# Optimization experiments

Measured on AMD Instinct MI355X. Metric: run time of the kernel, lower is better.

Reference implementation:

```python
import jax, jax.numpy as jnp
import numpy as np

EMBED_DIM = 1024
NUM_HEADS = 16
HEAD_DIM = EMBED_DIM // NUM_HEADS


def setup_inputs() -> dict:
    key = jax.random.key(0)
    k_x, k_wqkv, k_bqkv, k_wo, k_bo = jax.random.split(key, 5)
    B, T, C = 8, 1024, EMBED_DIM
    s = 1.0 / np.sqrt(C)
    return {
        "x": jax.random.normal(k_x, (B, T, C), dtype=jnp.float32),
        "W_qkv": jax.random.uniform(k_wqkv, (C, 3 * C), minval=-s, maxval=s, dtype=jnp.float32),
        "b_qkv": jax.random.uniform(k_bqkv, (3 * C,), minval=-s, maxval=s, dtype=jnp.float32),
        "W_out": jax.random.uniform(k_wo, (C, C), minval=-s, maxval=s, dtype=jnp.float32),
        "b_out": jax.random.uniform(k_bo, (C,), minval=-s, maxval=s, dtype=jnp.float32),
    }


def reference(x, W_qkv, b_qkv, W_out, b_out):
    B, T, C = x.shape
    H, D = NUM_HEADS, HEAD_DIM
    qkv = x @ W_qkv + b_qkv                      # [B,T,3C]
    q, k, v = jnp.split(qkv, 3, axis=-1)
    q = q.reshape(B, T, H, D).transpose(0, 2, 1, 3)  # [B,H,T,D]
    k = k.reshape(B, T, H, D).transpose(0, 2, 1, 3)
    v = v.reshape(B, T, H, D).transpose(0, 2, 1, 3)
    scores = jnp.einsum("bhqd,bhkd->bhqk", q, k) / np.sqrt(D).astype(np.float32)
    causal = jnp.tril(jnp.ones((T, T), dtype=bool))
    scores = jnp.where(causal[None, None], scores, -jnp.inf)
    attn = jax.nn.softmax(scores, axis=-1)       # dropout is identity in eval
    out = jnp.einsum("bhqk,bhkd->bhqd", attn, v)
    out = out.transpose(0, 2, 1, 3).reshape(B, T, C)
    return out @ W_out + b_out
```

## Files before the change

kernel.cpp:

```cpp
#include <hip/hip_runtime.h>
#include <hip/hip_bf16.h>
#include <cstdint>

using bf16 = __hip_bfloat16;
typedef short short8 __attribute__((ext_vector_type(8)));
typedef float floatx4 __attribute__((ext_vector_type(4)));

#define QSCALE 0.1803368801111601f

__device__ __forceinline__ void async_load16(const bf16* g, bf16* l) {
    __builtin_amdgcn_global_load_lds(
        (const __attribute__((address_space(1))) uint32_t*)g,
        (__attribute__((address_space(3))) uint32_t*)l, 16, 0, 0);
}

__device__ __forceinline__ void bar_lgkm0() {
    asm volatile("s_waitcnt lgkmcnt(0)\ns_barrier" ::: "memory");
}
__device__ __forceinline__ void bar_vm4() {
    asm volatile("s_waitcnt vmcnt(4)\ns_barrier" ::: "memory");
}
__device__ __forceinline__ void bar_vm0() {
    asm volatile("s_waitcnt vmcnt(0)\ns_barrier" ::: "memory");
}

__device__ __forceinline__ uint32_t pack2(float a, float b) {
    union { bf16 h[2]; uint32_t u; } p;
    p.h[0] = __float2bfloat16(a);
    p.h[1] = __float2bfloat16(b);
    return p.u;
}

__global__ __launch_bounds__(256)
void cvt_bf16_kernel(const float* __restrict__ in, bf16* __restrict__ out) {
    const int i = (blockIdx.x * 256 + threadIdx.x) * 4;
    const float4 v = *(const float4*)(in + i);
    bf16 o[4] = {__float2bfloat16(v.x), __float2bfloat16(v.y),
                 __float2bfloat16(v.z), __float2bfloat16(v.w)};
    *(ushort4*)(out + i) = *(ushort4*)o;
}

__global__ __launch_bounds__(256)
void transpose_cvt_kernel(const float* __restrict__ in, bf16* __restrict__ out,
                          int R, int C) {
    __shared__ float tile[32][33];
    const int tx = threadIdx.x & 31, ty = threadIdx.x >> 5;
    const int c0 = blockIdx.x * 32, r0 = blockIdx.y * 32;
    #pragma unroll
    for (int i = 0; i < 32; i += 8)
        tile[ty + i][tx] = in[(size_t)(r0 + ty + i) * C + c0 + tx];
    __syncthreads();
    #pragma unroll
    for (int i = 0; i < 32; i += 8)
        out[(size_t)(c0 + ty + i) * R + r0 + tx] = __float2bfloat16(tile[tx][ty + i]);
}

template <int MODE>
__global__ __launch_bounds__(256, 4)
void gemm_bt_kernel(const bf16* __restrict__ A, const bf16* __restrict__ Bt,
                    const float* __restrict__ bias, int K,
                    bf16* __restrict__ q_ws, bf16* __restrict__ k_ws,
                    bf16* __restrict__ vt_ws, float* __restrict__ out, int N) {
    __shared__ bf16 As[2][128 * 32];
    __shared__ bf16 Bs[2][128 * 32];
    const int tid = threadIdx.x;
    const int wave = tid >> 6, lane = tid & 63;
    const int ln = lane & 15, quad = lane >> 4;
    const int wm = wave & 1, wn = wave >> 1;
    const int m0 = blockIdx.y * 128, n0 = blockIdx.x * 128;

    floatx4 acc[4][4] = {};
    const int nkt = K >> 5;

    #pragma unroll
    for (int c = 0; c < 2; ++c) {
        const int e = (c * 256 + tid) * 8;
        async_load16(A + (size_t)(m0 + (e >> 5)) * K + (e & 31),
                     &As[0][(c * 256 + wave * 64) * 8]);
    }
    #pragma unroll
    for (int c = 0; c < 2; ++c) {
        const int e = (c * 256 + tid) * 8;
        async_load16(Bt + (size_t)(n0 + (e >> 5)) * K + (e & 31),
                     &Bs[0][(c * 256 + wave * 64) * 8]);
    }

    for (int kt = 0; kt < nkt; ++kt) {
        const int cur = kt & 1;
        bar_lgkm0();
        if (kt + 1 < nkt) {
            const int k0 = (kt + 1) << 5;
            #pragma unroll
            for (int c = 0; c < 2; ++c) {
                const int e = (c * 256 + tid) * 8;
                async_load16(A + (size_t)(m0 + (e >> 5)) * K + k0 + (e & 31),
                             &As[cur ^ 1][(c * 256 + wave * 64) * 8]);
            }
            #pragma unroll
            for (int c = 0; c < 2; ++c) {
                const int e = (c * 256 + tid) * 8;
                async_load16(Bt + (size_t)(n0 + (e >> 5)) * K + k0 + (e & 31),
                             &Bs[cur ^ 1][(c * 256 + wave * 64) * 8]);
            }
            bar_vm4();
        } else {
            bar_vm0();
        }

        short8 af[4], bfr[4];
        #pragma unroll
        for (int i = 0; i < 4; ++i) {
            af[i]  = *(const short8*)&As[cur][(wm * 64 + i * 16 + ln) * 32 + quad * 8];
            bfr[i] = *(const short8*)&Bs[cur][(wn * 64 + i * 16 + ln) * 32 + quad * 8];
        }
        #pragma unroll
        for (int mi = 0; mi < 4; ++mi)
            #pragma unroll
            for (int ni = 0; ni < 4; ++ni)
                acc[mi][ni] = __builtin_amdgcn_mfma_f32_16x16x32_bf16(
                    af[mi], bfr[ni], acc[mi][ni], 0, 0, 0);
    }

    #pragma unroll
    for (int ni = 0; ni < 4; ++ni) {
        const int col = n0 + wn * 64 + ni * 16 + ln;
        const float bv = bias[col];
        if (MODE == 0) {
            const int which = col >> 10;
            const int cc = col & 1023;
            const int h = cc >> 6, d = cc & 63;
            #pragma unroll
            for (int mi = 0; mi < 4; ++mi) {
                const int rowb = m0 + wm * 64 + mi * 16 + quad * 4;
                if (which == 2) {
                    const int bb = rowb >> 10, t = rowb & 1023;
                    const int tl = t & 63;
                    const int tt = (t & ~63) + ((((tl >> 3) ^ (d & 7)) << 3) | (tl & 7));
                    uint2 w2 = { pack2(acc[mi][ni][0] + bv, acc[mi][ni][1] + bv),
                                 pack2(acc[mi][ni][2] + bv, acc[mi][ni][3] + bv) };
                    *(uint2*)&vt_ws[((size_t)(bb * 16 + h) * 64 + d) * 1024 + tt] = w2;
                } else {
                    bf16* dst = (which == 0) ? q_ws : k_ws;
                    #pragma unroll
                    for (int r = 0; r < 4; ++r) {
                        const int row = rowb + r;
                        const int bb = row >> 10, t = row & 1023;
                        float v = acc[mi][ni][r] + bv;
                        if (which == 0) v *= QSCALE;
                        const int dd = (((d >> 3) ^ (t & 7)) << 3) | (d & 7);
                        dst[((size_t)(bb * 16 + h) * 1024 + t) * 64 + dd] =
                            __float2bfloat16(v);
                    }
                }
            }
        } else {
            #pragma unroll
            for (int mi = 0; mi < 4; ++mi) {
                const int rowb = m0 + wm * 64 + mi * 16 + quad * 4;
                #pragma unroll
                for (int r = 0; r < 4; ++r)
                    out[(size_t)(rowb + r) * N + col] = acc[mi][ni][r] + bv;
            }
        }
    }
}

__global__ __launch_bounds__(256, 4)
void attn_kernel(const bf16* __restrict__ Q, const bf16* __restrict__ K,
                 const bf16* __restrict__ Vt, bf16* __restrict__ O) {
    constexpr int T = 1024;
    __shared__ bf16 QPs[64 * 64];
    __shared__ bf16 Ks[2][64 * 64];
    __shared__ bf16 Vts[2][64 * 64];

    const int bh = blockIdx.y;
    const int tid = threadIdx.x;
    const int wave = tid >> 6, lane = tid & 63;
    const int ln = lane & 15, quad = lane >> 4;

    const bf16* Kg = K + (size_t)bh * T * 64;
    const bf16* Vg = Vt + (size_t)bh * 64 * T;
    const int b = bh >> 4, h = bh & 15;

    #pragma unroll
    for (int phase = 0; phase < 2; ++phase) {
        const int jt = phase ? 15 - blockIdx.x : blockIdx.x;
        const int q0 = jt * 64;
        const int nkt = jt + 1;

        bar_lgkm0();

        const bf16* Qg = Q + (size_t)bh * T * 64 + (size_t)q0 * 64;
        #pragma unroll
        for (int c = 0; c < 2; ++c)
            async_load16(Qg + (size_t)(c * 256 + tid) * 8,
                         &QPs[(c * 256 + wave * 64) * 8]);
        #pragma unroll
        for (int c = 0; c < 2; ++c)
            async_load16(Kg + (size_t)(c * 256 + tid) * 8,
                         &Ks[0][(c * 256 + wave * 64) * 8]);
        #pragma unroll
        for (int c = 0; c < 2; ++c) {
            const int e = (c * 256 + tid) * 8;
            async_load16(Vg + (size_t)(e >> 6) * T + (e & 63),
                         &Vts[0][(c * 256 + wave * 64) * 8]);
        }
        bar_vm0();

        short8 bq[2];
        #pragma unroll
        for (int ks = 0; ks < 2; ++ks) {
            const int row = wave * 16 + ln;
            const int ch = (ks * 4 + quad) ^ (row & 7);
            bq[ks] = *(const short8*)&QPs[row * 64 + ch * 8];
        }

        floatx4 oacc[4] = {};
        float rl = 0.f;
        const int qbw = q0 + wave * 16;

        for (int kt = 0; kt < nkt; ++kt) {
            const int cur = kt & 1;
            bar_lgkm0();
            if (kt + 1 < nkt) {
                const int nxt = cur ^ 1;
                #pragma unroll
                for (int c = 0; c < 2; ++c)
                    async_load16(Kg + (size_t)(kt + 1) * 4096 + (size_t)(c * 256 + tid) * 8,
                                 &Ks[nxt][(c * 256 + wave * 64) * 8]);
                #pragma unroll
                for (int c = 0; c < 2; ++c) {
                    const int e = (c * 256 + tid) * 8;
                    async_load16(Vg + (size_t)(e >> 6) * T + (kt + 1) * 64 + (e & 63),
                                 &Vts[nxt][(c * 256 + wave * 64) * 8]);
                }
                bar_vm4();
            } else {
                bar_vm0();
            }

            const int k0 = kt * 64;
            if (k0 > qbw + 15) continue;
            const bool tail = (k0 + 63 > qbw);

            floatx4 sacc[4] = {};
            #pragma unroll
            for (int nj = 0; nj < 4; ++nj) {
                if (tail && k0 + nj * 16 > qbw + 15) continue;
                #pragma unroll
                for (int ks = 0; ks < 2; ++ks) {
                    const int row = nj * 16 + ln;
                    const int ch = (ks * 4 + quad) ^ (row & 7);
                    const short8 ak = *(const short8*)&Ks[cur][row * 64 + ch * 8];
                    sacc[nj] = __builtin_amdgcn_mfma_f32_16x16x32_bf16(
                        ak, bq[ks], sacc[nj], 0, 0, 0);
                }
            }

            if (tail) {
                const int qq = qbw + ln;
                #pragma unroll
                for (int nj = 0; nj < 4; ++nj)
                    #pragma unroll
                    for (int r = 0; r < 4; ++r) {
                        const int kk = k0 + nj * 16 + quad * 4 + r;
                        if (kk > qq) sacc[nj][r] = -1e30f;
                    }
            }

            {
                float rs = 0.f;
                const int qrow = wave * 16 + ln;
                #pragma unroll
                for (int nj = 0; nj < 4; ++nj) {
                    float p[4];
                    #pragma unroll
                    for (int r = 0; r < 4; ++r) {
                        p[r] = exp2f(sacc[nj][r]);
                        rs += p[r];
                    }
                    const int kcol = nj * 16 + quad * 4;
                    const int ch = (kcol >> 3) ^ (qrow & 7);
                    uint2 w2 = { pack2(p[0], p[1]), pack2(p[2], p[3]) };
                    *(uint2*)&QPs[qrow * 64 + ch * 8 + (kcol & 7)] = w2;
                }
                rl += rs;
            }

            #pragma unroll
            for (int ks4 = 0; ks4 < 2; ++ks4) {
                const int qrow = wave * 16 + ln;
                const int chp = (ks4 * 4 + quad) ^ (qrow & 7);
                const short8 bp = *(const short8*)&QPs[qrow * 64 + chp * 8];
                #pragma unroll
                for (int dt = 0; dt < 4; ++dt) {
                    const int row = dt * 16 + ln;
                    const int ch = (ks4 * 4 + quad) ^ (row & 7);
                    const short8 av = *(const short8*)&Vts[cur][row * 64 + ch * 8];
                    oacc[dt] = __builtin_amdgcn_mfma_f32_16x16x32_bf16(
                        av, bp, oacc[dt], 0, 0, 0);
                }
            }
        }

        {
            float l = rl;
            l += __shfl_xor(l, 16, 64);
            l += __shfl_xor(l, 32, 64);
            const float inv = 1.0f / l;
            const int t = q0 + wave * 16 + ln;
            const size_t rowb = ((size_t)b * 1024 + t) * 1024 + h * 64;
            #pragma unroll
            for (int dt = 0; dt < 4; ++dt) {
                uint2 w2 = { pack2(oacc[dt][0] * inv, oacc[dt][1] * inv),
                             pack2(oacc[dt][2] * inv, oacc[dt][3] * inv) };
                *(uint2*)&O[rowb + dt * 16 + quad * 4] = w2;
            }
        }
    }
}

extern "C" void kernel_launch(void* const* d_in, const int* in_sizes, int n_in,
                              void* d_out, int out_size, void* d_ws, size_t ws_size,
                              hipStream_t stream) {
    const float* x     = (const float*)d_in[0];
    const float* W_qkv = (const float*)d_in[1];
    const float* b_qkv = (const float*)d_in[2];
    const float* W_out = (const float*)d_in[3];
    const float* b_out = (const float*)d_in[4];
    float* out = (float*)d_out;

    char* ws = (char*)d_ws;
    const size_t MB = 1u << 20;
    bf16* x_bf   = (bf16*)(ws + 0);
    bf16* wqkv_t = (bf16*)(ws + 16 * MB);
    bf16* wout_t = (bf16*)(ws + 22 * MB);
    bf16* q_ws   = (bf16*)(ws + 24 * MB);
    bf16* k_ws   = (bf16*)(ws + 40 * MB);
    bf16* vt_ws  = (bf16*)(ws + 56 * MB);
    bf16* ao_ws  = (bf16*)(ws + 72 * MB);

    cvt_bf16_kernel<<<8192, 256, 0, stream>>>(x, x_bf);
    transpose_cvt_kernel<<<dim3(96, 32), 256, 0, stream>>>(W_qkv, wqkv_t, 1024, 3072);
    transpose_cvt_kernel<<<dim3(32, 32), 256, 0, stream>>>(W_out, wout_t, 1024, 1024);

    gemm_bt_kernel<0><<<dim3(24, 64), 256, 0, stream>>>(
        x_bf, wqkv_t, b_qkv, 1024, q_ws, k_ws, vt_ws, nullptr, 3072);

    attn_kernel<<<dim3(8, 128), 256, 0, stream>>>(q_ws, k_ws, vt_ws, ao_ws);

    gemm_bt_kernel<1><<<dim3(8, 64), 256, 0, stream>>>(
        ao_ws, wout_t, b_out, 1024, nullptr, nullptr, nullptr, out, 1024);
}
```

Baseline: 250.7 us.

## Triple-buffer GEMM shared-memory tiles to prefetch two k-steps ahead

Converts the bf16 GEMM's double-buffered LDS pipeline into a three-stage ring that prefetches two k-tiles ahead. It also merges the two barriers per iteration into one combined vmcnt/lgkmcnt wait plus barrier. The aim is to hide more global-load latency and remove one barrier per k-step. In exchange, LDS use grows by half and the occupancy hint drops from 4 to 3 blocks per CU.

```diff
diff --git a/kernel.cpp b/kernel.cpp
--- a/kernel.cpp
+++ b/kernel.cpp
@@ -22,6 +22,12 @@
 }
 __device__ __forceinline__ void bar_vm0() {
     asm volatile("s_waitcnt vmcnt(0)\ns_barrier" ::: "memory");
+}
+__device__ __forceinline__ void bar_vm4_lgkm0() {
+    asm volatile("s_waitcnt vmcnt(4) lgkmcnt(0)\ns_barrier" ::: "memory");
+}
+__device__ __forceinline__ void bar_vm0_lgkm0() {
+    asm volatile("s_waitcnt vmcnt(0) lgkmcnt(0)\ns_barrier" ::: "memory");
 }
 
 __device__ __forceinline__ uint32_t pack2(float a, float b) {
@@ -56,13 +62,13 @@
 }
 
 template <int MODE>
-__global__ __launch_bounds__(256, 4)
+__global__ __launch_bounds__(256, 3)
 void gemm_bt_kernel(const bf16* __restrict__ A, const bf16* __restrict__ Bt,
                     const float* __restrict__ bias, int K,
                     bf16* __restrict__ q_ws, bf16* __restrict__ k_ws,
                     bf16* __restrict__ vt_ws, float* __restrict__ out, int N) {
-    __shared__ bf16 As[2][128 * 32];
-    __shared__ bf16 Bs[2][128 * 32];
+    __shared__ bf16 As[3][128 * 32];
+    __shared__ bf16 Bs[3][128 * 32];
     const int tid = threadIdx.x;
     const int wave = tid >> 6, lane = tid & 63;
     const int ln = lane & 15, quad = lane >> 4;
@@ -73,38 +79,42 @@
     const int nkt = K >> 5;
 
     #pragma unroll
-    for (int c = 0; c < 2; ++c) {
-        const int e = (c * 256 + tid) * 8;
-        async_load16(A + (size_t)(m0 + (e >> 5)) * K + (e & 31),
-                     &As[0][(c * 256 + wave * 64) * 8]);
+    for (int t = 0; t < 2; ++t) {
+        const int k0 = t << 5;
+        #pragma unroll
+        for (int c = 0; c < 2; ++c) {
+            const int e = (c * 256 + tid) * 8;
+            async_load16(A + (size_t)(m0 + (e >> 5)) * K + k0 + (e & 31),
+                         &As[t][(c * 256 + wave * 64) * 8]);
+        }
+        #pragma unroll
+        for (int c = 0; c < 2; ++c) {
+            const int e = (c * 256 + tid) * 8;
+            async_load16(Bt + (size_t)(n0 + (e >> 5)) * K + k0 + (e & 31),
+                         &Bs[t][(c * 256 + wave * 64) * 8]);
+        }
     }
-    #pragma unroll
-    for (int c = 0; c < 2; ++c) {
-        const int e = (c * 256 + tid) * 8;
-        async_load16(Bt + (size_t)(n0 + (e >> 5)) * K + (e & 31),
-                     &Bs[0][(c * 256 + wave * 64) * 8]);
-    }
 
     for (int kt = 0; kt < nkt; ++kt) {
-        const int cur = kt & 1;
-        bar_lgkm0();
-        if (kt + 1 < nkt) {
-            const int k0 = (kt + 1) << 5;
+        const int cur = kt % 3;
+        if (kt + 1 < nkt) bar_vm4_lgkm0();
+        else              bar_vm0_lgkm0();
+
+        if (kt + 2 < nkt) {
+            const int nxt = (kt + 2) % 3;
+            const int k0 = (kt + 2) << 5;
             #pragma unroll
             for (int c = 0; c < 2; ++c) {
                 const int e = (c * 256 + tid) * 8;
                 async_load16(A + (size_t)(m0 + (e >> 5)) * K + k0 + (e & 31),
-                             &As[cur ^ 1][(c * 256 + wave * 64) * 8]);
+                             &As[nxt][(c * 256 + wave * 64) * 8]);
             }
             #pragma unroll
             for (int c = 0; c < 2; ++c) {
                 const int e = (c * 256 + tid) * 8;
                 async_load16(Bt + (size_t)(n0 + (e >> 5)) * K + k0 + (e & 31),
-                             &Bs[cur ^ 1][(c * 256 + wave * 64) * 8]);
-            }
-            bar_vm4();
-        } else {
-            bar_vm0();
+                             &Bs[nxt][(c * 256 + wave * 64) * 8]);
+            }
         }
 
         short8 af[4], bfr[4];
```

Result: no change. 248.4 us (-0.9%).
